# Performance work log

Hardware: AMD Instinct MI355X
Metric: run time of the kernel (lower is better)

Reference implementation:

```python
import jax, jax.numpy as jnp
import numpy as np

NPOINT = 2048  # N // stride


def sqdist(a, b):
    # a: [B,M,3], b: [B,N,3] -> squared euclidean distances [B,M,N] (== cdist(...)**2)
    return (jnp.sum(a * a, -1)[:, :, None] + jnp.sum(b * b, -1)[:, None, :]
            - 2.0 * jnp.einsum('bmc,bnc->bmn', a, b))


def farthest_point_sample(xyz, npoint):
    # xyz [B,N,3] -> int32 [B,npoint]; deterministic start at point 0
    B, N, _ = xyz.shape

    def step(carry, _):
        distance, farthest = carry
        centroid = jnp.take_along_axis(xyz, farthest[:, None, None], axis=1)  # [B,1,3]
        d = jnp.sum((xyz - centroid) ** 2, -1)                                # [B,N]
        distance = jnp.minimum(distance, d)
        nxt = jnp.argmax(distance, -1).astype(jnp.int32)
        return (distance, nxt), farthest

    init = (jnp.full((B, N), 1e10, xyz.dtype), jnp.zeros((B,), jnp.int32))
    _, idx = jax.lax.scan(step, init, None, length=npoint)
    return idx.T  # [B, npoint]


def ball_query(radius, k, xyz, new_xyz):
    # faithful to torch ball_query: mask out-of-radius as N, sort indices, take first k,
    # replace padding with the first valid neighbor
    B, N, _ = xyz.shape
    sqd = sqdist(new_xyz, xyz)                                   # [B,S,N]
    gi = jnp.where(sqd > radius ** 2, N, jnp.arange(N, dtype=jnp.int32))
    gi = jnp.sort(gi, axis=-1)[:, :, :k]                         # [B,S,k]
    first = gi[:, :, :1]
    return jnp.where(gi == N, first, gi)


def three_interpolation(points, features, query):
    # points [B,S,3], features [B,D,S], query [B,N,3] -> [B,D,N]
    d = sqdist(query, points)                                    # [B,N,S]
    neg, idx = jax.lax.top_k(-d, 3)                              # 3 smallest dists
    w = 1.0 / (-neg + 1e-8)
    w = w / jnp.sum(w, -1, keepdims=True)                        # [B,N,3]
    g = jnp.take_along_axis(features[:, :, None, :], idx[:, None, :, :], axis=3)  # [B,D,N,3]
    return jnp.sum(g * w[:, None, :, :], -1)


def setup_inputs() -> dict:
    key = jax.random.key(0)
    k1, k2, k3, k4 = jax.random.split(key, 4)
    xyz = jax.random.uniform(k1, (4, 8192, 3), dtype=jnp.float32)
    features = jax.random.normal(k2, (4, 64, 8192), dtype=jnp.float32)
    W1 = jax.random.normal(k3, (128, 67), dtype=jnp.float32) * 0.05   # (3+64)->128 pointwise conv
    W2 = jax.random.normal(k4, (128, 192), dtype=jnp.float32) * 0.05  # (64+128)->128 pointwise conv
    return {"xyz": xyz, "features": features, "W1": W1, "W2": W2}


def reference(xyz, features, W1, W2):
    RADIUS, K = 0.2, 16
    # --- set abstraction (SABlock): FPS -> ball query -> group -> conv -> maxpool ---
    sidx = farthest_point_sample(xyz, NPOINT)                        # [B,S]
    new_xyz = jnp.take_along_axis(xyz, sidx[:, :, None], axis=1)     # [B,S,3]
    nidx = ball_query(RADIUS, K, xyz, new_xyz)                       # [B,S,K]
    gxyz = jnp.take_along_axis(xyz[:, None, :, :], nidx[:, :, :, None], axis=2)  # [B,S,K,3]
    rel = gxyz - new_xyz[:, :, None, :]                              # relative coords
    gfeat = jnp.take_along_axis(features[:, :, None, :], nidx[:, None, :, :], axis=3)  # [B,D,S,K]
    grouped = jnp.concatenate([rel.transpose(0, 3, 1, 2), gfeat], axis=1)  # [B,3+D,S,K]
    h = jax.nn.relu(jnp.einsum('od,bdsk->bosk', W1, grouped))
    sub_x = jnp.max(h, -1)                                           # [B,O,S]
    # --- feature propagation (UpBlock): 3-NN interpolation back to N -> concat -> conv ---
    lerp = three_interpolation(new_xyz, sub_x, xyz)                  # [B,O,N]
    cat = jnp.concatenate([features, lerp], axis=1)                  # [B,D+O,N]
    return jax.nn.relu(jnp.einsum('od,bdn->bon', W2, cat))           # [B,O,N]
```

## Files before the change

### kernel.cpp

```cpp
#include <hip/hip_runtime.h>
#include <hip/hip_bf16.h>

#define BATCH 4
#define NPTS  8192
#define NSAMP 2048
#define NK    16
#define CFEAT 64
#define CG    67
#define CO1   128
#define CCAT  192
#define CO2   128

#define DEV __device__ __forceinline__

typedef float f32x2 __attribute__((ext_vector_type(2)));

DEV float n3(float x, float y, float z) {
    return __fadd_rn(__fadd_rn(__fmul_rn(x, x), __fmul_rn(y, y)), __fmul_rn(z, z));
}
DEV float dot3(float ax, float ay, float az, float bx, float by, float bz) {
    return __fmaf_rn(az, bz, __fmaf_rn(ay, by, __fmul_rn(ax, bx)));
}
DEV float sqd_expand(float an, float bn, float d) {
    return __fsub_rn(__fadd_rn(an, bn), __fmul_rn(2.0f, d));
}

DEV f32x2 pk_add(f32x2 a, f32x2 b) {
    f32x2 d;
    asm("v_pk_add_f32 %0, %1, %2" : "=v"(d) : "v"(a), "v"(b));
    return d;
}
DEV f32x2 pk_mul(f32x2 a, f32x2 b) {
    f32x2 d;
    asm("v_pk_mul_f32 %0, %1, %2" : "=v"(d) : "v"(a), "v"(b));
    return d;
}

#define DPPMAX(x, ctrl)                                                        \
    x = fmaxf(x, __int_as_float(__builtin_amdgcn_update_dpp(                   \
            __float_as_int(x), __float_as_int(x), (ctrl), 0xF, 0xF, false)))

__global__ __launch_bounds__(256) void transpose_kernel(const float* __restrict__ F,
                                                        float* __restrict__ T) {
    __shared__ float tile[64][65];
    const int b = blockIdx.y;
    const int n0 = blockIdx.x * 64;
    const int tx = threadIdx.x & 63, ty = threadIdx.x >> 6;
    const float* Fb = F + (size_t)b * CFEAT * NPTS;
    float* Tb = T + (size_t)b * NPTS * CFEAT;
#pragma unroll
    for (int i = 0; i < 16; i++) {
        int c = ty + i * 4;
        tile[c][tx] = Fb[(size_t)c * NPTS + n0 + tx];
    }
    __syncthreads();
#pragma unroll
    for (int i = 0; i < 16; i++) {
        int r = ty + i * 4;
        Tb[(size_t)(n0 + r) * CFEAT + tx] = tile[tx][r];
    }
}

__global__ __launch_bounds__(512, 2) void fps_kernel(const float* __restrict__ xyz,
                                                     float* __restrict__ new_xyz) {
    const int b = blockIdx.x;
    const int t = threadIdx.x;
    const int lane = t & 63, wv = t >> 6;
    const float* X = xyz + (size_t)b * NPTS * 3;

    __shared__ float sx[NPTS], sy[NPTS], sz[NPTS];
    __shared__ unsigned long long wred[2][8];

    f32x2 px[8], py[8], pz[8], dd[8];
    {
        const float4* X4 = (const float4*)X;
#pragma unroll
        for (int g = 0; g < 4; g++) {
            float4 f0 = X4[t * 12 + g * 3 + 0];
            float4 f1 = X4[t * 12 + g * 3 + 1];
            float4 f2 = X4[t * 12 + g * 3 + 2];
            px[2*g+0].x = f0.x; py[2*g+0].x = f0.y; pz[2*g+0].x = f0.z;
            px[2*g+0].y = f0.w; py[2*g+0].y = f1.x; pz[2*g+0].y = f1.y;
            px[2*g+1].x = f1.z; py[2*g+1].x = f1.w; pz[2*g+1].x = f2.x;
            px[2*g+1].y = f2.y; py[2*g+1].y = f2.z; pz[2*g+1].y = f2.w;
        }
#pragma unroll
        for (int j = 0; j < 8; j++) {
            int p = t * 16 + 2 * j;
            sx[p] = px[j].x; sy[p] = py[j].x; sz[p] = pz[j].x;
            sx[p + 1] = px[j].y; sy[p + 1] = py[j].y; sz[p + 1] = pz[j].y;
            dd[j].x = 1e10f; dd[j].y = 1e10f;
        }
    }
    __syncthreads();

    float cx = sx[0], cy = sy[0], cz = sz[0];
    if (t == 0) {
        size_t o = (size_t)b * NSAMP * 3;
        new_xyz[o + 0] = cx; new_xyz[o + 1] = cy; new_xyz[o + 2] = cz;
    }

    int par = 0;
    for (int s = 1; s < NSAMP; s++) {
        const float ncx = -cx, ncy = -cy, ncz = -cz;
        const f32x2 vcx = {ncx, ncx}, vcy = {ncy, ncy}, vcz = {ncz, ncz};
#pragma unroll
        for (int j = 0; j < 8; j++) {
            f32x2 dx = pk_add(px[j], vcx);
            f32x2 dy = pk_add(py[j], vcy);
            f32x2 dz = pk_add(pz[j], vcz);
            f32x2 d = pk_add(pk_add(pk_mul(dx, dx), pk_mul(dy, dy)), pk_mul(dz, dz));
            dd[j].x = fminf(dd[j].x, d.x);
            dd[j].y = fminf(dd[j].y, d.y);
        }
        float m[8];
#pragma unroll
        for (int j = 0; j < 8; j++) m[j] = fmaxf(dd[j].x, dd[j].y);
#pragma unroll
        for (int j = 0; j < 4; j++) m[j] = fmaxf(m[j], m[j + 4]);
        float bv = fmaxf(fmaxf(m[0], m[1]), fmaxf(m[2], m[3]));
        int bj = 15;
#pragma unroll
        for (int j = 14; j >= 0; --j) {
            float dj = (j & 1) ? dd[j >> 1].y : dd[j >> 1].x;
            if (dj == bv) bj = j;
        }
        const int lidx = t * 16 + bj;

        float wm = bv;
        DPPMAX(wm, 0x111);
        DPPMAX(wm, 0x112);
        DPPMAX(wm, 0x114);
        DPPMAX(wm, 0x118);
        DPPMAX(wm, 0x142);
        DPPMAX(wm, 0x143);
        const float wmax = __int_as_float(
            __builtin_amdgcn_readlane(__float_as_int(wm), 63));
        const unsigned long long em = __ballot(bv == wmax);
        const int wl = (int)__builtin_ctzll(em);
        const int widx = __builtin_amdgcn_readlane(lidx, wl);

        if (lane == 0)
            wred[par][wv] = ((unsigned long long)__float_as_uint(wmax) << 32)
                          | (unsigned int)(~widx);
        __syncthreads();

        unsigned long long r0 = wred[par][0], r1 = wred[par][1];
        unsigned long long r2 = wred[par][2], r3 = wred[par][3];
        unsigned long long r4 = wred[par][4], r5 = wred[par][5];
        unsigned long long r6 = wred[par][6], r7 = wred[par][7];
        if (r1 > r0) r0 = r1;
        if (r3 > r2) r2 = r3;
        if (r5 > r4) r4 = r5;
        if (r7 > r6) r6 = r7;
        if (r2 > r0) r0 = r2;
        if (r6 > r4) r4 = r6;
        if (r4 > r0) r0 = r4;
        const int idx = (int)(~(unsigned int)(r0 & 0xFFFFFFFFull));

        cx = sx[idx]; cy = sy[idx]; cz = sz[idx];
        if (t == 0) {
            size_t o = ((size_t)b * NSAMP + s) * 3;
            new_xyz[o + 0] = cx; new_xyz[o + 1] = cy; new_xyz[o + 2] = cz;
        }
        par ^= 1;
    }
}

__global__ __launch_bounds__(256) void ballq_kernel(const float* __restrict__ xyz,
                                                    const float* __restrict__ new_xyz,
                                                    int* __restrict__ nidx) {
    const int wv = threadIdx.x >> 6, lane = threadIdx.x & 63;
    const int q = blockIdx.x * 4 + wv;
    const int b = q >> 11;
    const float* X = xyz + (size_t)b * NPTS * 3;
    const float* Q = new_xyz + (size_t)q * 3;
    const float qx = Q[0], qy = Q[1], qz = Q[2];
    const float an = n3(qx, qy, qz);

    __shared__ int nb[4][NK];
    int cnt = 0;
    for (int base = 0; base < NPTS && cnt < NK; base += 64) {
        int p = base + lane;
        float x = X[p * 3 + 0], y = X[p * 3 + 1], z = X[p * 3 + 2];
        float bn = n3(x, y, z);
        float dt = dot3(qx, qy, qz, x, y, z);
        float sq = sqd_expand(an, bn, dt);
        bool in = (sq <= 0.04f);
        unsigned long long m = __ballot(in);
        if (in) {
            int pos = cnt + (int)__popcll(m & ((1ull << lane) - 1ull));
            if (pos < NK) nb[wv][pos] = p;
        }
        cnt += (int)__popcll(m);
    }
    __syncthreads();
    if (lane < NK) {
        int c = cnt < NK ? cnt : NK;
        int v = (lane < c) ? nb[wv][lane] : nb[wv][0];
        nidx[(size_t)q * NK + lane] = v;
    }
}

__global__ __launch_bounds__(256) void group_mlp_kernel(const float* __restrict__ xyz,
                                                        const float* __restrict__ featT,
                                                        const float* __restrict__ new_xyz,
                                                        const int* __restrict__ nidx,
                                                        const float* __restrict__ W1,
                                                        float* __restrict__ subxT) {
    __shared__ float w1t[CG * CO1];
    for (int i = threadIdx.x; i < CG * CO1; i += 256) {
        int d = i >> 7, o = i & 127;
        w1t[i] = W1[(size_t)o * CG + d];
    }
    __syncthreads();
    const int lane = threadIdx.x & 63, wv = threadIdx.x >> 6;

    for (int q = blockIdx.x * 4 + wv; q < BATCH * NSAMP; q += gridDim.x * 4) {
        const int b = q >> 11;
        const float* Q = new_xyz + (size_t)q * 3;
        const float qx = Q[0], qy = Q[1], qz = Q[2];
        const int* NB = nidx + (size_t)q * NK;
        float m0 = 0.0f, m1 = 0.0f;
#pragma unroll 1
        for (int k = 0; k < NK; k++) {
            const int n = NB[k];
            const float* P = xyz + ((size_t)b * NPTS + n) * 3;
            float rx = P[0] - qx, ry = P[1] - qy, rz = P[2] - qz;
            float fv = featT[((size_t)b * NPTS + n) * CFEAT + lane];
            float a0 = fmaf(w1t[0 * CO1 + lane], rx,
                       fmaf(w1t[1 * CO1 + lane], ry, w1t[2 * CO1 + lane] * rz));
            float a1 = fmaf(w1t[0 * CO1 + 64 + lane], rx,
                       fmaf(w1t[1 * CO1 + 64 + lane], ry, w1t[2 * CO1 + 64 + lane] * rz));
#pragma unroll
            for (int d = 3; d < CG; d++) {
                float g = __shfl(fv, d - 3);
                a0 = fmaf(w1t[d * CO1 + lane], g, a0);
                a1 = fmaf(w1t[d * CO1 + 64 + lane], g, a1);
            }
            m0 = fmaxf(m0, a0);
            m1 = fmaxf(m1, a1);
        }
        subxT[(size_t)q * CO1 + lane] = m0;
        subxT[(size_t)q * CO1 + 64 + lane] = m1;
    }
}

DEV void ins3(float dd, int jj,
              float& d0, int& i0, float& d1, int& i1, float& d2, int& i2) {
    bool c2 = (dd < d2) || (dd == d2 && jj < i2);
    if (c2) { d2 = dd; i2 = jj; }
    bool c1 = (d2 < d1) || (d2 == d1 && i2 < i1);
    if (c1) { float tv = d1; int ti = i1; d1 = d2; i1 = i2; d2 = tv; i2 = ti; }
    bool c0 = (d1 < d0) || (d1 == d0 && i1 < i0);
    if (c0) { float tv = d0; int ti = i0; d0 = d1; i0 = i1; d1 = tv; i1 = ti; }
}

__global__ __launch_bounds__(256) void interp_w2_kernel(const float* __restrict__ xyz,
                                                        const float* __restrict__ new_xyz,
                                                        const float* __restrict__ featT,
                                                        const float* __restrict__ subxT,
                                                        const float* __restrict__ W2,
                                                        float* __restrict__ out) {
    __shared__ float w2t[CCAT * CO2];
    __shared__ float catb[4][CCAT];
    for (int i = threadIdx.x; i < CCAT * CO2; i += 256) {
        int d = i >> 7, o = i & 127;
        w2t[i] = W2[(size_t)o * CCAT + d];
    }
    __syncthreads();
    const int lane = threadIdx.x & 63, wv = threadIdx.x >> 6;

    for (int q = blockIdx.x * 4 + wv; q < BATCH * NPTS; q += gridDim.x * 4) {
        const int b = q >> 13, n = q & (NPTS - 1);
        const float* P = xyz + (size_t)q * 3;
        const float qx = P[0], qy = P[1], qz = P[2];
        const float an = n3(qx, qy, qz);

        float d0 = 1e30f, d1 = 1e30f, d2 = 1e30f;
        int i0 = 0x7fffffff, i1 = 0x7fffffff, i2 = 0x7fffffff;
        for (int j = lane; j < NSAMP; j += 64) {
            const float* C = new_xyz + ((size_t)b * NSAMP + j) * 3;
            float x = C[0], y = C[1], z = C[2];
            float bn = n3(x, y, z);
            float dt = dot3(qx, qy, qz, x, y, z);
            float dd = sqd_expand(an, bn, dt);
            ins3(dd, j, d0, i0, d1, i1, d2, i2);
        }
#pragma unroll
        for (int off = 32; off > 0; off >>= 1) {
            float e0 = __shfl_xor(d0, off); int f0 = __shfl_xor(i0, off);
            float e1 = __shfl_xor(d1, off); int f1 = __shfl_xor(i1, off);
            float e2 = __shfl_xor(d2, off); int f2 = __shfl_xor(i2, off);
            ins3(e0, f0, d0, i0, d1, i1, d2, i2);
            ins3(e1, f1, d0, i0, d1, i1, d2, i2);
            ins3(e2, f2, d0, i0, d1, i1, d2, i2);
        }
        float w0 = 1.0f / (d0 + 1e-8f);
        float w1 = 1.0f / (d1 + 1e-8f);
        float w2 = 1.0f / (d2 + 1e-8f);
        float sw = (w0 + w1) + w2;
        w0 /= sw; w1 /= sw; w2 /= sw;

        const float* S = subxT + (size_t)b * NSAMP * CO1;
        float L0 = S[(size_t)i0 * CO1 + lane] * w0
                 + S[(size_t)i1 * CO1 + lane] * w1
                 + S[(size_t)i2 * CO1 + lane] * w2;
        float L1 = S[(size_t)i0 * CO1 + 64 + lane] * w0
                 + S[(size_t)i1 * CO1 + 64 + lane] * w1
                 + S[(size_t)i2 * CO1 + 64 + lane] * w2;

        float fv = featT[((size_t)b * NPTS + n) * CFEAT + lane];
        catb[wv][lane] = fv;
        catb[wv][64 + lane] = L0;
        catb[wv][128 + lane] = L1;
        __builtin_amdgcn_s_waitcnt(0);

        float a0 = 0.0f, a1 = 0.0f;
#pragma unroll 8
        for (int d = 0; d < CCAT; d++) {
            float cv = catb[wv][d];
            a0 = fmaf(w2t[d * CO2 + lane], cv, a0);
            a1 = fmaf(w2t[d * CO2 + 64 + lane], cv, a1);
        }
        out[((size_t)b * CO2 + lane) * NPTS + n] = fmaxf(a0, 0.0f);
        out[((size_t)b * CO2 + 64 + lane) * NPTS + n] = fmaxf(a1, 0.0f);
    }
}

extern "C" void kernel_launch(void* const* d_in, const int* in_sizes, int n_in,
                              void* d_out, int out_size, void* d_ws, size_t ws_size,
                              hipStream_t stream) {
    const float* xyz      = (const float*)d_in[0];
    const float* features = (const float*)d_in[1];
    const float* W1       = (const float*)d_in[2];
    const float* W2       = (const float*)d_in[3];
    float* out = (float*)d_out;

    float* featT   = (float*)d_ws;
    float* new_xyz = featT + (size_t)BATCH * NPTS * CFEAT;
    int*   nidx    = (int*)(new_xyz + (size_t)BATCH * NSAMP * 3);
    float* subxT   = (float*)(nidx + (size_t)BATCH * NSAMP * NK);

    transpose_kernel<<<dim3(NPTS / 64, BATCH), 256, 0, stream>>>(features, featT);
    fps_kernel<<<BATCH, 512, 0, stream>>>(xyz, new_xyz);
    ballq_kernel<<<(BATCH * NSAMP) / 4, 256, 0, stream>>>(xyz, new_xyz, nidx);
    group_mlp_kernel<<<512, 256, 0, stream>>>(xyz, featT, new_xyz, nidx, W1, subxT);
    interp_w2_kernel<<<256, 256, 0, stream>>>(xyz, new_xyz, featT, subxT, W2, out);
}
```

Measured before the change: 2.539 ms.

## Use readlane broadcasts, paired weight layout, and DPP cross-wave reduction across kernels

In FPS, the serial 8-way cross-wave argmax is replaced by a DPP-based 64-bit max across lanes, and xy coordinates are packed into one LDS array. The group MLP and interp/W2 kernels now store transposed weights as float2 pairs so each lane gets both output channels in one LDS read. They broadcast activations with readlane instead of shfl or an LDS staging buffer. The group MLP also processes two neighbors per iteration to reuse weight loads. Trade-off: higher register pressure and larger unrolled code in exchange for fewer LDS accesses and shuffles in the FPS-dominated pipeline.

```diff
diff --git a/kernel.cpp b/kernel.cpp
--- a/kernel.cpp
+++ b/kernel.cpp
@@ -40,6 +40,19 @@
     x = fmaxf(x, __int_as_float(__builtin_amdgcn_update_dpp(                   \
             __float_as_int(x), __float_as_int(x), (ctrl), 0xF, 0xF, false)))
 
+template <int CTRL>
+DEV void dpp_shr_max64(unsigned& hi, unsigned& lo) {
+    unsigned nh = (unsigned)__builtin_amdgcn_update_dpp((int)hi, (int)hi, CTRL, 0xF, 0xF, false);
+    unsigned nl = (unsigned)__builtin_amdgcn_update_dpp((int)lo, (int)lo, CTRL, 0xF, 0xF, false);
+    unsigned long long a = ((unsigned long long)hi << 32) | lo;
+    unsigned long long n = ((unsigned long long)nh << 32) | nl;
+    if (n > a) { hi = nh; lo = nl; }
+}
+
+DEV float rlane(float v, int l) {
+    return __int_as_float(__builtin_amdgcn_readlane(__float_as_int(v), l));
+}
+
 __global__ __launch_bounds__(256) void transpose_kernel(const float* __restrict__ F,
                                                         float* __restrict__ T) {
     __shared__ float tile[64][65];
@@ -68,7 +81,8 @@
     const int lane = t & 63, wv = t >> 6;
     const float* X = xyz + (size_t)b * NPTS * 3;
 
-    __shared__ float sx[NPTS], sy[NPTS], sz[NPTS];
+    __shared__ f32x2 sxy[NPTS];
+    __shared__ float szl[NPTS];
     __shared__ unsigned long long wred[2][8];
 
     f32x2 px[8], py[8], pz[8], dd[8];
@@ -87,14 +101,15 @@
 #pragma unroll
         for (int j = 0; j < 8; j++) {
             int p = t * 16 + 2 * j;
-            sx[p] = px[j].x; sy[p] = py[j].x; sz[p] = pz[j].x;
-            sx[p + 1] = px[j].y; sy[p + 1] = py[j].y; sz[p + 1] = pz[j].y;
+            sxy[p].x = px[j].x; sxy[p].y = py[j].x; szl[p] = pz[j].x;
+            sxy[p+1].x = px[j].y; sxy[p+1].y = py[j].y; szl[p+1] = pz[j].y;
             dd[j].x = 1e10f; dd[j].y = 1e10f;
         }
     }
     __syncthreads();
 
-    float cx = sx[0], cy = sy[0], cz = sz[0];
+    f32x2 c0 = sxy[0];
+    float cx = c0.x, cy = c0.y, cz = szl[0];
     if (t == 0) {
         size_t o = (size_t)b * NSAMP * 3;
         new_xyz[o + 0] = cx; new_xyz[o + 1] = cy; new_xyz[o + 2] = cz;
@@ -145,20 +160,16 @@
                           | (unsigned int)(~widx);
         __syncthreads();
 
-        unsigned long long r0 = wred[par][0], r1 = wred[par][1];
-        unsigned long long r2 = wred[par][2], r3 = wred[par][3];
-        unsigned long long r4 = wred[par][4], r5 = wred[par][5];
-        unsigned long long r6 = wred[par][6], r7 = wred[par][7];
-        if (r1 > r0) r0 = r1;
-        if (r3 > r2) r2 = r3;
-        if (r5 > r4) r4 = r5;
-        if (r7 > r6) r6 = r7;
-        if (r2 > r0) r0 = r2;
-        if (r6 > r4) r4 = r6;
-        if (r4 > r0) r0 = r4;
-        const int idx = (int)(~(unsigned int)(r0 & 0xFFFFFFFFull));
-
-        cx = sx[idx]; cy = sy[idx]; cz = sz[idx];
+        unsigned long long v = wred[par][lane & 7];
+        unsigned hi = (unsigned)(v >> 32), lo = (unsigned)v;
+        dpp_shr_max64<0x111>(hi, lo);
+        dpp_shr_max64<0x112>(hi, lo);
+        dpp_shr_max64<0x114>(hi, lo);
+        const int idx = ~__builtin_amdgcn_readlane((int)lo, 7);
+
+        f32x2 cxy = sxy[idx];
+        cz = szl[idx];
+        cx = cxy.x; cy = cxy.y;
         if (t == 0) {
             size_t o = ((size_t)b * NSAMP + s) * 3;
             new_xyz[o + 0] = cx; new_xyz[o + 1] = cy; new_xyz[o + 2] = cz;
@@ -208,10 +219,11 @@
                                                         const int* __restrict__ nidx,
                                                         const float* __restrict__ W1,
                                                         float* __restrict__ subxT) {
-    __shared__ float w1t[CG * CO1];
-    for (int i = threadIdx.x; i < CG * CO1; i += 256) {
-        int d = i >> 7, o = i & 127;
-        w1t[i] = W1[(size_t)o * CG + d];
+    __shared__ f32x2 w1t2[CG][64];
+    for (int i = threadIdx.x; i < CG * 64; i += 256) {
+        int d = i >> 6, o = i & 63;
+        w1t2[d][o].x = W1[(size_t)o * CG + d];
+        w1t2[d][o].y = W1[(size_t)(o + 64) * CG + d];
     }
     __syncthreads();
     const int lane = threadIdx.x & 63, wv = threadIdx.x >> 6;
@@ -223,23 +235,31 @@
         const int* NB = nidx + (size_t)q * NK;
         float m0 = 0.0f, m1 = 0.0f;
 #pragma unroll 1
-        for (int k = 0; k < NK; k++) {
-            const int n = NB[k];
-            const float* P = xyz + ((size_t)b * NPTS + n) * 3;
-            float rx = P[0] - qx, ry = P[1] - qy, rz = P[2] - qz;
-            float fv = featT[((size_t)b * NPTS + n) * CFEAT + lane];
-            float a0 = fmaf(w1t[0 * CO1 + lane], rx,
-                       fmaf(w1t[1 * CO1 + lane], ry, w1t[2 * CO1 + lane] * rz));
-            float a1 = fmaf(w1t[0 * CO1 + 64 + lane], rx,
-                       fmaf(w1t[1 * CO1 + 64 + lane], ry, w1t[2 * CO1 + 64 + lane] * rz));
-#pragma unroll
-            for (int d = 3; d < CG; d++) {
-                float g = __shfl(fv, d - 3);
-                a0 = fmaf(w1t[d * CO1 + lane], g, a0);
-                a1 = fmaf(w1t[d * CO1 + 64 + lane], g, a1);
+        for (int k = 0; k < NK; k += 2) {
+            const int n0 = NB[k], n1 = NB[k + 1];
+            const float* P0 = xyz + ((size_t)b * NPTS + n0) * 3;
+            const float* P1 = xyz + ((size_t)b * NPTS + n1) * 3;
+            float rx0 = P0[0] - qx, ry0 = P0[1] - qy, rz0 = P0[2] - qz;
+            float rx1 = P1[0] - qx, ry1 = P1[1] - qy, rz1 = P1[2] - qz;
+            float fv0 = featT[((size_t)b * NPTS + n0) * CFEAT + lane];
+            float fv1 = featT[((size_t)b * NPTS + n1) * CFEAT + lane];
+            f32x2 w0 = w1t2[0][lane], w1 = w1t2[1][lane], w2 = w1t2[2][lane];
+            float a0 = fmaf(w0.x, rx0, fmaf(w1.x, ry0, w2.x * rz0));
+            float a1 = fmaf(w0.y, rx0, fmaf(w1.y, ry0, w2.y * rz0));
+            float c0 = fmaf(w0.x, rx1, fmaf(w1.x, ry1, w2.x * rz1));
+            float c1 = fmaf(w0.y, rx1, fmaf(w1.y, ry1, w2.y * rz1));
+#pragma unroll
+            for (int c = 0; c < 64; c++) {
+                f32x2 w = w1t2[3 + c][lane];
+                float g0 = rlane(fv0, c);
+                float g1 = rlane(fv1, c);
+                a0 = fmaf(w.x, g0, a0);
+                a1 = fmaf(w.y, g0, a1);
+                c0 = fmaf(w.x, g1, c0);
+                c1 = fmaf(w.y, g1, c1);
             }
-            m0 = fmaxf(m0, a0);
-            m1 = fmaxf(m1, a1);
+            m0 = fmaxf(m0, fmaxf(a0, c0));
+            m1 = fmaxf(m1, fmaxf(a1, c1));
         }
         subxT[(size_t)q * CO1 + lane] = m0;
         subxT[(size_t)q * CO1 + 64 + lane] = m1;
@@ -262,11 +282,11 @@
                                                         const float* __restrict__ subxT,
                                                         const float* __restrict__ W2,
                                                         float* __restrict__ out) {
-    __shared__ float w2t[CCAT * CO2];
-    __shared__ float catb[4][CCAT];
-    for (int i = threadIdx.x; i < CCAT * CO2; i += 256) {
-        int d = i >> 7, o = i & 127;
-        w2t[i] = W2[(size_t)o * CCAT + d];
+    __shared__ f32x2 w2t2[CCAT][64];
+    for (int i = threadIdx.x; i < CCAT * 64; i += 256) {
+        int d = i >> 6, o = i & 63;
+        w2t2[d][o].x = W2[(size_t)o * CCAT + d];
+        w2t2[d][o].y = W2[(size_t)(o + 64) * CCAT + d];
     }
     __syncthreads();
     const int lane = threadIdx.x & 63, wv = threadIdx.x >> 6;
@@ -311,17 +331,25 @@
                  + S[(size_t)i2 * CO1 + 64 + lane] * w2;
 
         float fv = featT[((size_t)b * NPTS + n) * CFEAT + lane];
-        catb[wv][lane] = fv;
-        catb[wv][64 + lane] = L0;
-        catb[wv][128 + lane] = L1;
-        __builtin_amdgcn_s_waitcnt(0);
 
         float a0 = 0.0f, a1 = 0.0f;
-#pragma unroll 8
-        for (int d = 0; d < CCAT; d++) {
-            float cv = catb[wv][d];
-            a0 = fmaf(w2t[d * CO2 + lane], cv, a0);
-            a1 = fmaf(w2t[d * CO2 + 64 + lane], cv, a1);
+#pragma unroll
+        for (int c = 0; c < 64; c++) {
+            f32x2 w = w2t2[c][lane];
+            float g = rlane(fv, c);
+            a0 = fmaf(w.x, g, a0); a1 = fmaf(w.y, g, a1);
+        }
+#pragma unroll
+        for (int c = 0; c < 64; c++) {
+            f32x2 w = w2t2[64 + c][lane];
+            float g = rlane(L0, c);
+            a0 = fmaf(w.x, g, a0); a1 = fmaf(w.y, g, a1);
+        }
+#pragma unroll
+        for (int c = 0; c < 64; c++) {
+            f32x2 w = w2t2[128 + c][lane];
+            float g = rlane(L1, c);
+            a0 = fmaf(w.x, g, a0); a1 = fmaf(w.y, g, a1);
         }
         out[((size_t)b * CO2 + lane) * NPTS + n] = fmaxf(a0, 0.0f);
         out[((size_t)b * CO2 + 64 + lane) * NPTS + n] = fmaxf(a1, 0.0f);
```

Measured after the change: 2.512 ms. About the same (-1.1%).
